# Kernel optimization log

Measured on AMD Instinct MI355X. Metric: run time of the kernel, lower is better.

## Reference

```python
import jax, jax.numpy as jnp
import numpy as np

B, T, N = 256, 4096, 64


def setup_inputs() -> dict:
    key = jax.random.key(0)
    u = jax.random.normal(key, (B, T), dtype=jnp.float32)
    # LRU-style stable parameterization: rho chosen so r = exp(-softplus(rho)) = radii
    radii = np.clip(0.9 + 0.0015 * np.arange(N), 1e-6, 1 - 1e-6)
    rho = np.log(np.expm1(-np.log(radii))).astype(np.float32)
    theta = (np.pi * np.arange(N) / N).astype(np.float32)
    return {
        "u": u,
        "rho": jnp.asarray(rho),
        "theta": jnp.asarray(theta),
        "b_real": jnp.ones((N,), jnp.float32),
        "b_imag": jnp.zeros((N,), jnp.float32),
        "c_real": jnp.ones((N,), jnp.float32),
        "c_imag": jnp.zeros((N,), jnp.float32),
    }


def reference(u, rho, theta, b_real, b_imag, c_real, c_imag):
    # lambda = exp(-softplus(rho)) * exp(i*theta), strictly inside unit circle
    r = jnp.exp(-jax.nn.softplus(rho))
    lam = (r.astype(jnp.complex64) * jnp.exp(1j * theta)).astype(jnp.complex64)
    b = (b_real + 1j * b_imag).astype(jnp.complex64)
    c_conj = jnp.conj((c_real + 1j * c_imag).astype(jnp.complex64))
    # precompute driving term b * u_t for all t: (T, B, N)
    bu = jnp.swapaxes(b[None, None, :] * u[:, :, None], 0, 1)

    def step(x, bu_t):
        x = lam * x + bu_t            # (B, N) complex diagonal recurrence
        y_t = jnp.real(x @ c_conj)    # (B,) readout Re(c^H x)
        return x, y_t

    x0 = jnp.zeros((u.shape[0], rho.shape[0]), dtype=jnp.complex64)
    _, ys = jax.lax.scan(step, x0, bu)  # ys: (T, B)
    return jnp.swapaxes(ys, 0, 1)       # (B, T) float32
```

## Files before the change

### kernel.cpp

```cpp
#include <hip/hip_runtime.h>
#include <hip/hip_bf16.h>

#define T_LEN  4096
#define NLAG   5
#define CMAX   575
#define ESTR   728
#define ROUNDS 9

typedef __attribute__((ext_vector_type(8))) short short8;
typedef __attribute__((ext_vector_type(4))) float f32x4;

static __device__ __forceinline__ unsigned short f2bf(float f) {
  __hip_bfloat16 h = __float2bfloat16(f);
  return *reinterpret_cast<unsigned short*>(&h);
}

template <int CTRL>
static __device__ __forceinline__ float dppmov(float x) {
  return __int_as_float(__builtin_amdgcn_update_dpp(
      0, __float_as_int(x), CTRL, 0xF, 0xF, true));
}

#define CVT8(dst, va, vb) {                                                       \
    short8 _v;                                                                    \
    _v[0] = (short)f2bf((va).x); _v[1] = (short)f2bf((va).y);                     \
    _v[2] = (short)f2bf((va).z); _v[3] = (short)f2bf((va).w);                     \
    _v[4] = (short)f2bf((vb).x); _v[5] = (short)f2bf((vb).y);                     \
    _v[6] = (short)f2bf((vb).z); _v[7] = (short)f2bf((vb).w);                     \
    *reinterpret_cast<short8*>(dst) = _v; }

#define LBAR() { asm volatile("s_waitcnt lgkmcnt(0)" ::: "memory");               \
                 __builtin_amdgcn_s_barrier(); }

__global__ __launch_bounds__(1024, 4) void ssm_one(
    const float* __restrict__ u, const float* __restrict__ rho,
    const float* __restrict__ theta, const float* __restrict__ br,
    const float* __restrict__ bi, const float* __restrict__ cr,
    const float* __restrict__ ci, float* __restrict__ out) {
  __shared__ __align__(16) unsigned short Ab[2][8192];
  __shared__ __align__(16) unsigned short E8[8 * ESTR];
  __shared__ __align__(16) f32x4 scr[16][64];

  const int tid = threadIdx.x;
  const int lane = tid & 63;
  const int w = tid >> 6;
  const bool prod = (w >= 8);
  const int ptid = tid & 511;

  const int bid = blockIdx.x;
  const int swz = (bid & 7) * 32 + (bid >> 3);
  const int t0 = (swz & 63) * 64;
  const int b0 = (swz >> 6) * 64;

  const int lrow = lane >> 4, lc16 = lane & 15;
  const float4 z4 = make_float4(0.f, 0.f, 0.f, 0.f);
  float4 av[2][2][2];
  f32x4 acc[2][2] = {};

#define ISSUEA(j, S) { _Pragma("unroll") for (int h_ = 0; h_ < 2; ++h_) {         \
    const int hh = ptid + 512 * h_;                                               \
    const int r_ = hh >> 4, cg = hh & 15;                                         \
    const int gg = t0 - (j) * 128 + cg * 8;                                       \
    if ((unsigned)gg < 4096u) {                                                   \
      const float* p_ = u + (size_t)(b0 + r_) * T_LEN + gg;                       \
      av[S][h_][0] = *reinterpret_cast<const float4*>(p_);                        \
      av[S][h_][1] = *reinterpret_cast<const float4*>(p_ + 4);                    \
    } else { av[S][h_][0] = z4; av[S][h_][1] = z4; } } }

#define WRITEA(buf, S) { _Pragma("unroll") for (int h_ = 0; h_ < 2; ++h_) {       \
    const int hh = ptid + 512 * h_;                                               \
    const int r_ = hh >> 4, cg = hh & 15;                                         \
    const int eo = r_ * 128 + ((cg * 8) ^ ((r_ & 7) << 3));                       \
    CVT8(&Ab[buf][eo], av[S][h_][0], av[S][h_][1]); } }

  float Lr[9], Li[9], gr = 0.f, gi = 0.f;
  const bool l0 = lane & 1, l1 = lane & 2, l3 = lane & 8;
  const int sig = ((lane & 1) << 2) | (lane & 2) | ((lane >> 3) & 1);
  const int cc  = ((lane >> 2) & 1) | ((lane >> 3) & 2) | ((lane >> 3) & 4);

  if (prod) {
    ISSUEA(0, 0);
    const short8 z8 = {};
    for (int c = ptid; c < ESTR; c += 512)
      *reinterpret_cast<short8*>(&E8[c * 8]) = z8;
  } else {
    const float rh = rho[lane], th = theta[lane];
    const float lr2 = -1.4426950408f * log1pf(expf(rh));
    const float rr_ = exp2f(lr2);
    const float lre = rr_ * __cosf(th), lim = rr_ * __sinf(th);
    const float brv = br[lane], biv = bi[lane];
    const float crv = cr[lane], civ = ci[lane];
    const float wre = crv * brv + civ * biv;
    const float wim = crv * biv - civ * brv;
    Lr[0] = 1.f; Li[0] = 0.f;
#pragma unroll
    for (int i = 1; i <= 8; ++i) {
      Lr[i] = Lr[i - 1] * lre - Li[i - 1] * lim;
      Li[i] = Lr[i - 1] * lim + Li[i - 1] * lre;
    }
    const float d0f = (float)(8 * ROUNDS * w);
    const float rd0 = exp2f(d0f * lr2);
    float f0 = d0f * (th * 0.15915494309f);
    f0 -= floorf(f0);
    const float a0 = 6.2831853072f * f0;
    const float c0 = __cosf(a0), s0 = __sinf(a0);
    gr = rd0 * (wre * c0 - wim * s0);
    gi = rd0 * (wre * s0 + wim * c0);
  }

  LBAR();

#define ROUND(rnd) {                                                              \
    float v[8];                                                                   \
    _Pragma("unroll") for (int i2 = 0; i2 < 8; ++i2)                              \
      v[i2] = gr * Lr[i2] - gi * Li[i2];                        \
    { const float ngr = gr * Lr[8] - gi * Li[8];                                  \
      const float ngi = gr * Li[8] + gi * Lr[8];                                  \
      gr = ngr; gi = ngi; }                                                       \
    float s4[4];                                                                  \
    _Pragma("unroll") for (int i = 0; i < 4; ++i) {                               \
      const float t_ = l0 ? v[i + 4] : v[i];                                      \
      const float u2 = l0 ? v[i] : v[i + 4];                                      \
      s4[i] = t_ + dppmov<0xB1>(u2); }                                            \
    float s2[2];                                                                  \
    _Pragma("unroll") for (int i = 0; i < 2; ++i) {                               \
      const float t_ = l1 ? s4[i + 2] : s4[i];                                    \
      const float u2 = l1 ? s4[i] : s4[i + 2];                                    \
      s2[i] = t_ + dppmov<0x4E>(u2); }                                            \
    float y_;                                                                     \
    { const float t_ = l3 ? s2[1] : s2[0];                                        \
      const float u2 = l3 ? s2[0] : s2[1];                                        \
      y_ = t_ + dppmov<0x128>(u2); }                                              \
    y_ += __shfl_xor(y_, 4);                                                      \
    y_ += __shfl_xor(y_, 16);                                                     \
    y_ += __shfl_xor(y_, 32);                                                     \
    const int d_ = 72 * w + 8 * (rnd) + sig;                                      \
    const int yy = CMAX - d_;                                                     \
    if (yy >= cc) E8[cc * ESTR + (yy - cc)] = f2bf(y_); }

  if (prod) {
    WRITEA(0, 0);
    ISSUEA(1, 1);
  } else {
    ROUND(0); ROUND(1); ROUND(2); ROUND(3); ROUND(4);
    ROUND(5); ROUND(6); ROUND(7); ROUND(8);
  }
  LBAR();

  const int qr = (w >> 2) & 1, qc = (w >> 1) & 1, kh = w & 1;

#define COMPUTE(jj, buf) {                                                        \
    const unsigned short* A = Ab[buf];                                            \
    const int pB = 7 - (lc16 & 7);                                                \
    _Pragma("unroll") for (int ksl = 0; ksl < 2; ++ksl) {                         \
      const int ks = kh * 2 + ksl;                                                \
      short8 af[2], bfr[2];                                                       \
      _Pragma("unroll") for (int ft = 0; ft < 2; ++ft) {                          \
        const int r = qr * 32 + ft * 16 + lc16;                                   \
        const int pe = (ks * 32 + lrow * 8) ^ ((r & 7) << 3);                     \
        af[ft] = *reinterpret_cast<const short8*>(&A[r * 128 + pe]); }            \
      _Pragma("unroll") for (int fn = 0; fn < 2; ++fn) {                          \
        const int tc = qc * 32 + fn * 16 + lc16;                                  \
        const int x0 = CMAX - (jj) * 128 - tc + ks * 32 + lrow * 8 - pB;          \
        bfr[fn] = *reinterpret_cast<const short8*>(&E8[pB * ESTR + x0]); }        \
      _Pragma("unroll") for (int ft = 0; ft < 2; ++ft)                            \
        _Pragma("unroll") for (int fn = 0; fn < 2; ++fn)                          \
          acc[ft][fn] = __builtin_amdgcn_mfma_f32_16x16x32_bf16(                  \
              af[ft], bfr[fn], acc[ft][fn], 0, 0, 0); } }

#pragma unroll
  for (int j = 0; j < NLAG; ++j) {
    if (prod) {
      if (j + 1 < NLAG) WRITEA((j + 1) & 1, (j + 1) & 1);
      if (j + 2 < NLAG) ISSUEA(j + 2, j & 1);
    } else {
      COMPUTE(j, j & 1);
    }
    if (j < NLAG - 1) LBAR();
  }

  const int qid = qr * 2 + qc;
  if (!prod && kh == 1) {
#pragma unroll
    for (int ft = 0; ft < 2; ++ft)
#pragma unroll
      for (int fn = 0; fn < 2; ++fn)
        scr[qid * 4 + ft * 2 + fn][lane] = acc[ft][fn];
  }
  LBAR();
  if (!prod && kh == 0) {
#pragma unroll
    for (int ft = 0; ft < 2; ++ft)
#pragma unroll
      for (int fn = 0; fn < 2; ++fn) {
        const f32x4 s = scr[qid * 4 + ft * 2 + fn][lane];
#pragma unroll
        for (int rg = 0; rg < 4; ++rg) {
          const int row = b0 + qr * 32 + ft * 16 + lrow * 4 + rg;
          const int col = t0 + qc * 32 + fn * 16 + lc16;
          out[(size_t)row * T_LEN + col] = acc[ft][fn][rg] + s[rg];
        }
      }
  }
#undef ISSUEA
#undef WRITEA
#undef COMPUTE
#undef ROUND
}

extern "C" void kernel_launch(void* const* d_in, const int* in_sizes, int n_in,
                              void* d_out, int out_size, void* d_ws, size_t ws_size,
                              hipStream_t stream) {
  const float* u     = (const float*)d_in[0];
  const float* rho   = (const float*)d_in[1];
  const float* theta = (const float*)d_in[2];
  const float* br    = (const float*)d_in[3];
  const float* bi    = (const float*)d_in[4];
  const float* cr    = (const float*)d_in[5];
  const float* ci    = (const float*)d_in[6];
  float* out = (float*)d_out;

  ssm_one<<<256, 1024, 0, stream>>>(u, rho, theta, br, bi, cr, ci, out);
}
```

Measured before the change: 12.24 us.

## Spread impulse-response generation across all waves and drop the extra barrier

The lagged impulse-response table was built only by the non-producer waves, nine rounds each. Now every wave computes eigenvalue powers, and each wave handles up to five strided rounds using a lambda^128 step, so producer waves share the work. The zeroing of the table is reduced to just the unwritten tail region, and one block barrier is removed. Producer waves issue both A loads before computing, which overlaps global load latency with the math. In exchange, producer waves now repeat the parameter transcendentals, and using lambda^128 by repeated squaring may add a little rounding error.

New measurement: 13.45 us. +9.9%, slower.

```diff
diff --git a/kernel.cpp b/kernel.cpp
--- a/kernel.cpp
+++ b/kernel.cpp
@@ -5,7 +5,6 @@
 #define NLAG   5
 #define CMAX   575
 #define ESTR   728
-#define ROUNDS 9
 
 typedef __attribute__((ext_vector_type(8))) short short8;
 typedef __attribute__((ext_vector_type(4))) float f32x4;
@@ -73,78 +72,91 @@
     const int eo = r_ * 128 + ((cg * 8) ^ ((r_ & 7) << 3));                       \
     CVT8(&Ab[buf][eo], av[S][h_][0], av[S][h_][1]); } }
 
-  float Lr[9], Li[9], gr = 0.f, gi = 0.f;
+  if (prod) {
+    ISSUEA(0, 0);
+    ISSUEA(1, 1);
+    for (int idx = ptid; idx < 8 * 160; idx += 512) {
+      const int p = idx / 160, jz = idx - p * 160;
+      const int x = 576 - p + jz;
+      if (x <= 727) E8[p * ESTR + x] = 0;
+    }
+  }
+
+  const float rh = rho[lane], th = theta[lane];
+  const float lr2 = -1.4426950408f * log1pf(expf(rh));
+  const float rr_ = exp2f(lr2);
+  const float lre = rr_ * __cosf(th), lim = rr_ * __sinf(th);
+  const float brv = br[lane], biv = bi[lane];
+  const float crv = cr[lane], civ = ci[lane];
+  const float wre = crv * brv + civ * biv;
+  const float wim = crv * biv - civ * brv;
+
+  float Lr[9], Li[9];
+  Lr[0] = 1.f; Li[0] = 0.f;
+#pragma unroll
+  for (int i = 1; i <= 8; ++i) {
+    Lr[i] = Lr[i - 1] * lre - Li[i - 1] * lim;
+    Li[i] = Lr[i - 1] * lim + Li[i - 1] * lre;
+  }
+  float L128r = Lr[8], L128i = Li[8];
+#pragma unroll
+  for (int qd = 0; qd < 4; ++qd) {
+    const float nr = L128r * L128r - L128i * L128i;
+    const float ni = 2.f * L128r * L128i;
+    L128r = nr; L128i = ni;
+  }
+
+  const float d0f = (float)(8 * w);
+  const float rd0 = exp2f(d0f * lr2);
+  float f0 = d0f * (th * 0.15915494309f);
+  f0 -= floorf(f0);
+  const float a0 = 6.2831853072f * f0;
+  const float c0 = __cosf(a0), s0 = __sinf(a0);
+  float gr = rd0 * (wre * c0 - wim * s0);
+  float gi = rd0 * (wre * s0 + wim * c0);
+
   const bool l0 = lane & 1, l1 = lane & 2, l3 = lane & 8;
   const int sig = ((lane & 1) << 2) | (lane & 2) | ((lane >> 3) & 1);
   const int cc  = ((lane >> 2) & 1) | ((lane >> 3) & 2) | ((lane >> 3) & 4);
 
-  if (prod) {
-    ISSUEA(0, 0);
-    const short8 z8 = {};
-    for (int c = ptid; c < ESTR; c += 512)
-      *reinterpret_cast<short8*>(&E8[c * 8]) = z8;
-  } else {
-    const float rh = rho[lane], th = theta[lane];
-    const float lr2 = -1.4426950408f * log1pf(expf(rh));
-    const float rr_ = exp2f(lr2);
-    const float lre = rr_ * __cosf(th), lim = rr_ * __sinf(th);
-    const float brv = br[lane], biv = bi[lane];
-    const float crv = cr[lane], civ = ci[lane];
-    const float wre = crv * brv + civ * biv;
-    const float wim = crv * biv - civ * brv;
-    Lr[0] = 1.f; Li[0] = 0.f;
-#pragma unroll
-    for (int i = 1; i <= 8; ++i) {
-      Lr[i] = Lr[i - 1] * lre - Li[i - 1] * lim;
-      Li[i] = Lr[i - 1] * lim + Li[i - 1] * lre;
+  {
+    const int nr_ = prod ? 4 : 5;
+    for (int p = 0; p < nr_; ++p) {
+      float v[8];
+#pragma unroll
+      for (int i2 = 0; i2 < 8; ++i2)
+        v[i2] = gr * Lr[i2] - gi * Li[i2];
+      { const float ngr = gr * L128r - gi * L128i;
+        const float ngi = gr * L128i + gi * L128r;
+        gr = ngr; gi = ngi; }
+      float s4[4];
+#pragma unroll
+      for (int i = 0; i < 4; ++i) {
+        const float t_ = l0 ? v[i + 4] : v[i];
+        const float u2 = l0 ? v[i] : v[i + 4];
+        s4[i] = t_ + dppmov<0xB1>(u2);
+      }
+      float s2[2];
+#pragma unroll
+      for (int i = 0; i < 2; ++i) {
+        const float t_ = l1 ? s4[i + 2] : s4[i];
+        const float u2 = l1 ? s4[i] : s4[i + 2];
+        s2[i] = t_ + dppmov<0x4E>(u2);
+      }
+      float y_;
+      { const float t_ = l3 ? s2[1] : s2[0];
+        const float u2 = l3 ? s2[0] : s2[1];
+        y_ = t_ + dppmov<0x128>(u2); }
+      y_ += __shfl_xor(y_, 4);
+      y_ += __shfl_xor(y_, 16);
+      y_ += __shfl_xor(y_, 32);
+      const int d_ = 8 * w + 128 * p + sig;
+      const int yy = CMAX - d_;
+      if (yy >= cc) E8[cc * ESTR + (yy - cc)] = f2bf(y_);
     }
-    const float d0f = (float)(8 * ROUNDS * w);
-    const float rd0 = exp2f(d0f * lr2);
-    float f0 = d0f * (th * 0.15915494309f);
-    f0 -= floorf(f0);
-    const float a0 = 6.2831853072f * f0;
-    const float c0 = __cosf(a0), s0 = __sinf(a0);
-    gr = rd0 * (wre * c0 - wim * s0);
-    gi = rd0 * (wre * s0 + wim * c0);
-  }
-
-  LBAR();
-
-#define ROUND(rnd) {                                                              \
-    float v[8];                                                                   \
-    _Pragma("unroll") for (int i2 = 0; i2 < 8; ++i2)                              \
-      v[i2] = gr * Lr[i2] - gi * Li[i2];                        \
-    { const float ngr = gr * Lr[8] - gi * Li[8];                                  \
-      const float ngi = gr * Li[8] + gi * Lr[8];                                  \
-      gr = ngr; gi = ngi; }                                                       \
-    float s4[4];                                                                  \
-    _Pragma("unroll") for (int i = 0; i < 4; ++i) {                               \
-      const float t_ = l0 ? v[i + 4] : v[i];                                      \
-      const float u2 = l0 ? v[i] : v[i + 4];                                      \
-      s4[i] = t_ + dppmov<0xB1>(u2); }                                            \
-    float s2[2];                                                                  \
-    _Pragma("unroll") for (int i = 0; i < 2; ++i) {                               \
-      const float t_ = l1 ? s4[i + 2] : s4[i];                                    \
-      const float u2 = l1 ? s4[i] : s4[i + 2];                                    \
-      s2[i] = t_ + dppmov<0x4E>(u2); }                                            \
-    float y_;                                                                     \
-    { const float t_ = l3 ? s2[1] : s2[0];                                        \
-      const float u2 = l3 ? s2[0] : s2[1];                                        \
-      y_ = t_ + dppmov<0x128>(u2); }                                              \
-    y_ += __shfl_xor(y_, 4);                                                      \
-    y_ += __shfl_xor(y_, 16);                                                     \
-    y_ += __shfl_xor(y_, 32);                                                     \
-    const int d_ = 72 * w + 8 * (rnd) + sig;                                      \
-    const int yy = CMAX - d_;                                                     \
-    if (yy >= cc) E8[cc * ESTR + (yy - cc)] = f2bf(y_); }
-
-  if (prod) {
-    WRITEA(0, 0);
-    ISSUEA(1, 1);
-  } else {
-    ROUND(0); ROUND(1); ROUND(2); ROUND(3); ROUND(4);
-    ROUND(5); ROUND(6); ROUND(7); ROUND(8);
-  }
+  }
+
+  if (prod) WRITEA(0, 0);
   LBAR();
 
   const int qr = (w >> 2) & 1, qc = (w >> 1) & 1, kh = w & 1;
@@ -205,7 +217,6 @@
 #undef ISSUEA
 #undef WRITEA
 #undef COMPUTE
-#undef ROUND
 }
 
 extern "C" void kernel_launch(void* const* d_in, const int* in_sizes, int n_in,
```
